# Performance work log

Measured on AMD Instinct MI355X. Metric: run time of the kernel, lower is better.

The kernel has to match this reference:

```python
import jax, jax.numpy as jnp
import numpy as np

TOP_K = 2


def setup_inputs() -> dict:
    key = jax.random.key(0)
    k1, k2, k3, k4, k5 = jax.random.split(key, 5)
    B, S, D, F, E = 2, 2048, 1024, 4096, 8
    hidden_states = jax.random.normal(k1, (B, S, D), dtype=jnp.float32)
    gate_w = jax.random.normal(k2, (E, D), dtype=jnp.float32) / np.sqrt(D)
    w1 = jax.random.normal(k3, (E, F, D), dtype=jnp.float32) / np.sqrt(D)
    w3 = jax.random.normal(k4, (E, F, D), dtype=jnp.float32) / np.sqrt(D)
    w2 = jax.random.normal(k5, (E, D, F), dtype=jnp.float32) / np.sqrt(F)
    return {"hidden_states": hidden_states, "gate_w": gate_w, "w1": w1, "w3": w3, "w2": w2}


def reference(hidden_states, gate_w, w1, w3, w2):
    B, S, D = hidden_states.shape
    E = gate_w.shape[0]
    x = hidden_states.reshape(-1, D)  # [T, D]
    # Router: softmax in float32, top-k, renormalize (Mixtral gating)
    router_logits = x @ gate_w.T  # [T, E]
    probs = jax.nn.softmax(router_logits.astype(jnp.float32), axis=-1)
    routing_weights, selected_experts = jax.lax.top_k(probs, TOP_K)  # [T, K]
    routing_weights = routing_weights / routing_weights.sum(axis=-1, keepdims=True)
    routing_weights = routing_weights.astype(x.dtype)
    out = jnp.zeros_like(x)
    for e in range(E):
        # combined routing weight of expert e for each token (0 if not routed)
        w = (routing_weights * (selected_experts == e)).sum(axis=-1)  # [T]
        h = jax.nn.silu(x @ w1[e].T) * (x @ w3[e].T)  # [T, F]
        out = out + (h @ w2[e].T) * w[:, None]
    return out.reshape(B, S, D)
```

## Files before the change

### kernel.cpp

```cpp
#include <hip/hip_runtime.h>
#include <hip/hip_bf16.h>
#include <stdint.h>

#define T_TOK 4096
#define D_DIM 1024
#define F_DIM 4096
#define E_NUM 8
#define MAXTOK 4096
#define TOTROW 8192

typedef __attribute__((ext_vector_type(8))) short short8;
typedef __attribute__((ext_vector_type(4))) float floatx4;

__device__ __forceinline__ unsigned short f2bf(float f) {
    union { float f; unsigned u; } v; v.f = f;
    unsigned u = v.u;
    u += 0x7fff + ((u >> 16) & 1);
    return (unsigned short)(u >> 16);
}

__device__ __forceinline__ void async_copy16(const unsigned short* g, unsigned short* l) {
    __builtin_amdgcn_global_load_lds(
        (__attribute__((address_space(1))) void*)(g),
        (__attribute__((address_space(3))) void*)(l), 16, 0, 0);
}

__global__ __launch_bounds__(256) void cvt_kernel(
    const float* __restrict__ src, unsigned short* __restrict__ dst, int n8)
{
    int i = blockIdx.x * blockDim.x + threadIdx.x;
    int stride = gridDim.x * blockDim.x;
    for (; i < n8; i += stride) {
        const float4* s = (const float4*)src + 2 * (size_t)i;
        float4 a = s[0], b = s[1];
        short8 o;
        o[0] = (short)f2bf(a.x); o[1] = (short)f2bf(a.y);
        o[2] = (short)f2bf(a.z); o[3] = (short)f2bf(a.w);
        o[4] = (short)f2bf(b.x); o[5] = (short)f2bf(b.y);
        o[6] = (short)f2bf(b.z); o[7] = (short)f2bf(b.w);
        *((short8*)dst + (size_t)i) = o;
    }
}

__global__ __launch_bounds__(64) void router_kernel(
    const float* __restrict__ x, const float* __restrict__ gw,
    int* __restrict__ counts, int* __restrict__ tok, float* __restrict__ rw,
    int* __restrict__ se, int* __restrict__ sp, float* __restrict__ sw)
{
    const int t = blockIdx.x;
    const int l = threadIdx.x;
    const float4* xr = (const float4*)(x + (size_t)t * D_DIM);
    float acc[E_NUM];
#pragma unroll
    for (int e = 0; e < E_NUM; e++) acc[e] = 0.f;
#pragma unroll
    for (int i = 0; i < D_DIM / 4 / 64; i++) {
        float4 xv = xr[l + i * 64];
#pragma unroll
        for (int e = 0; e < E_NUM; e++) {
            float4 gv = ((const float4*)(gw + e * D_DIM))[l + i * 64];
            acc[e] += xv.x * gv.x + xv.y * gv.y + xv.z * gv.z + xv.w * gv.w;
        }
    }
#pragma unroll
    for (int e = 0; e < E_NUM; e++) {
        float a = acc[e];
        for (int off = 32; off > 0; off >>= 1) a += __shfl_xor(a, off, 64);
        acc[e] = a;
    }
    if (l == 0) {
        int e0 = 0;
#pragma unroll
        for (int e = 1; e < E_NUM; e++) if (acc[e] > acc[e0]) e0 = e;
        int e1 = (e0 == 0) ? 1 : 0;
#pragma unroll
        for (int e = 0; e < E_NUM; e++) if (e != e0 && acc[e] > acc[e1]) e1 = e;
        float w0 = 1.f / (1.f + expf(acc[e1] - acc[e0]));
        float w1 = 1.f - w0;
        int p0 = atomicAdd(&counts[e0], 1);
        tok[e0 * MAXTOK + p0] = t; rw[e0 * MAXTOK + p0] = w0;
        int p1 = atomicAdd(&counts[e1], 1);
        tok[e1 * MAXTOK + p1] = t; rw[e1 * MAXTOK + p1] = w1;
        se[2 * t] = e0; sp[2 * t] = p0; sw[2 * t] = w0;
        se[2 * t + 1] = e1; sp[2 * t + 1] = p1; sw[2 * t + 1] = w1;
    }
}

__global__ void prefix_kernel(const int* __restrict__ counts, int* __restrict__ offsets)
{
    if (threadIdx.x == 0 && blockIdx.x == 0) {
        int run = 0;
        for (int e = 0; e < E_NUM; e++) { offsets[e] = run; run += counts[e]; }
    }
}


__global__ __launch_bounds__(256, 4) void gemm1f_kernel(
    const unsigned short* __restrict__ xb,
    const unsigned short* __restrict__ w1b, const unsigned short* __restrict__ w3b,
    const int* __restrict__ counts, const int* __restrict__ offsets,
    const int* __restrict__ tok, unsigned short* __restrict__ h)
{
    const int lin = blockIdx.x + 32 * (blockIdx.y + 64 * blockIdx.z);
    const int w = (lin & 7) * 2048 + (lin >> 3);
    const int tm = w & 31;
    const int tn = (w >> 5) & 63;
    const int e  = w >> 11;

    const int cnt = counts[e];
    if (tm * 128 >= cnt) return;
    const int tid = threadIdx.x;

    __shared__ unsigned short sA[2][128 * 32];
    __shared__ unsigned short sB1[2][64 * 32];
    __shared__ unsigned short sB3[2][64 * 32];
    __shared__ int tokS[128];

    if (tid < 128) {
        int r = tm * 128 + tid;
        tokS[tid] = tok[e * MAXTOK + (r < cnt ? r : cnt - 1)];
    }
    __syncthreads();

    const int wave = tid >> 6, lane = tid & 63;
    const int wx = wave & 1, wy = wave >> 1;
    const int quad = lane >> 4, tl = lane & 15;

    const int sr = tid >> 2;
    const int scw = ((tid & 3) ^ ((sr >> 1) & 3)) * 8;
    const unsigned offA0 = (unsigned)tokS[sr] * D_DIM + scw;
    const unsigned offA1 = (unsigned)tokS[sr + 64] * D_DIM + scw;
    const unsigned offB  = ((unsigned)e * F_DIM + (unsigned)tn * 64 + sr) * D_DIM + scw;

    const int l0 = wave * 512;
    const int l1 = 2048 + wave * 512;

    floatx4 acc1[4][2], acc3[4][2];
#pragma unroll
    for (int a = 0; a < 4; a++)
#pragma unroll
        for (int b = 0; b < 2; b++) {
            acc1[a][b] = (floatx4){0.f, 0.f, 0.f, 0.f};
            acc3[a][b] = (floatx4){0.f, 0.f, 0.f, 0.f};
        }

    async_copy16(xb + offA0, sA[0] + l0);
    async_copy16(xb + offA1, sA[0] + l1);
    async_copy16(w1b + offB, sB1[0] + l0);
    async_copy16(w3b + offB, sB3[0] + l0);
    __syncthreads();

    int cur = 0;
    for (int kk = 0; kk < D_DIM; kk += 32) {
        const int nk = kk + 32;
        if (nk < D_DIM) {
            async_copy16(xb + offA0 + nk, sA[cur ^ 1] + l0);
            async_copy16(xb + offA1 + nk, sA[cur ^ 1] + l1);
            async_copy16(w1b + offB + nk, sB1[cur ^ 1] + l0);
            async_copy16(w3b + offB + nk, sB3[cur ^ 1] + l0);
        }

        short8 af[4];
#pragma unroll
        for (int mt = 0; mt < 4; mt++) {
            const int ra = wy * 64 + mt * 16 + tl;
            af[mt] = *(const short8*)(sA[cur] + ra * 32 + (quad ^ ((ra >> 1) & 3)) * 8);
        }
#pragma unroll
        for (int nt = 0; nt < 2; nt++) {
            const int rb = wx * 32 + nt * 16 + tl;
            const int cb = (quad ^ ((rb >> 1) & 3)) * 8;
            short8 b1 = *(const short8*)(sB1[cur] + rb * 32 + cb);
            short8 b3 = *(const short8*)(sB3[cur] + rb * 32 + cb);
#pragma unroll
            for (int mt = 0; mt < 4; mt++) {
                acc1[mt][nt] = __builtin_amdgcn_mfma_f32_16x16x32_bf16(af[mt], b1, acc1[mt][nt], 0, 0, 0);
                acc3[mt][nt] = __builtin_amdgcn_mfma_f32_16x16x32_bf16(af[mt], b3, acc3[mt][nt], 0, 0, 0);
            }
        }
        __syncthreads();
        cur ^= 1;
    }

    const int hbase = offsets[e];
#pragma unroll
    for (int mt = 0; mt < 4; mt++)
#pragma unroll
        for (int nt = 0; nt < 2; nt++)
#pragma unroll
            for (int i = 0; i < 4; i++) {
                int r = tm * 128 + wy * 64 + mt * 16 + quad * 4 + i;
                if (r < cnt) {
                    int c = tn * 64 + wx * 32 + nt * 16 + tl;
                    float z1 = acc1[mt][nt][i];
                    float z3 = acc3[mt][nt][i];
                    float hv = (z1 / (1.f + expf(-z1))) * z3;
                    h[(size_t)(hbase + r) * F_DIM + c] = f2bf(hv);
                }
            }
}

__global__ __launch_bounds__(256, 4) void gemm2f_kernel(
    const unsigned short* __restrict__ h, const unsigned short* __restrict__ w2b,
    const int* __restrict__ counts, const int* __restrict__ offsets,
    float* __restrict__ hout)
{
    const int lin = blockIdx.x + 32 * (blockIdx.y + 8 * blockIdx.z);
    const int w = (lin & 7) * 256 + (lin >> 3);
    const int tm = w & 31;
    const int tn = (w >> 5) & 7;
    const int e  = w >> 8;

    const int cnt = counts[e];
    if (tm * 128 >= cnt) return;
    const int tid = threadIdx.x;

    __shared__ unsigned short sA[2][128 * 32];
    __shared__ unsigned short sB[2][128 * 32];

    const int hbase = offsets[e];
    const int wave = tid >> 6, lane = tid & 63;
    const int wx = wave & 1, wy = wave >> 1;
    const int quad = lane >> 4, tl = lane & 15;

    const int sr = tid >> 2;
    const int scw = ((tid & 3) ^ ((sr >> 1) & 3)) * 8;
    int ra0 = hbase + tm * 128 + sr;      if (ra0 > TOTROW - 1) ra0 = TOTROW - 1;
    int ra1 = ra0 + 64;                   if (ra1 > TOTROW - 1) ra1 = TOTROW - 1;
    const unsigned offA0 = (unsigned)ra0 * F_DIM + scw;
    const unsigned offA1 = (unsigned)ra1 * F_DIM + scw;
    const unsigned offB  = ((unsigned)e * D_DIM + (unsigned)tn * 128 + sr) * F_DIM + scw;
    const unsigned offB1 = offB + 64u * F_DIM;

    const int l0 = wave * 512;
    const int l1 = 2048 + wave * 512;

    floatx4 acc[4][4];
#pragma unroll
    for (int a = 0; a < 4; a++)
#pragma unroll
        for (int b = 0; b < 4; b++) acc[a][b] = (floatx4){0.f, 0.f, 0.f, 0.f};

    async_copy16(h + offA0, sA[0] + l0);
    async_copy16(h + offA1, sA[0] + l1);
    async_copy16(w2b + offB, sB[0] + l0);
    async_copy16(w2b + offB1, sB[0] + l1);
    __syncthreads();

    int cur = 0;
    for (int kk = 0; kk < F_DIM; kk += 32) {
        const int nk = kk + 32;
        if (nk < F_DIM) {
            async_copy16(h + offA0 + nk, sA[cur ^ 1] + l0);
            async_copy16(h + offA1 + nk, sA[cur ^ 1] + l1);
            async_copy16(w2b + offB + nk, sB[cur ^ 1] + l0);
            async_copy16(w2b + offB1 + nk, sB[cur ^ 1] + l1);
        }

        short8 af[4];
#pragma unroll
        for (int mt = 0; mt < 4; mt++) {
            const int ra = wy * 64 + mt * 16 + tl;
            af[mt] = *(const short8*)(sA[cur] + ra * 32 + (quad ^ ((ra >> 1) & 3)) * 8);
        }
#pragma unroll
        for (int nt = 0; nt < 4; nt++) {
            const int rb = wx * 64 + nt * 16 + tl;
            short8 bf = *(const short8*)(sB[cur] + rb * 32 + (quad ^ ((rb >> 1) & 3)) * 8);
#pragma unroll
            for (int mt = 0; mt < 4; mt++)
                acc[mt][nt] = __builtin_amdgcn_mfma_f32_16x16x32_bf16(af[mt], bf, acc[mt][nt], 0, 0, 0);
        }
        __syncthreads();
        cur ^= 1;
    }

#pragma unroll
    for (int mt = 0; mt < 4; mt++)
#pragma unroll
        for (int nt = 0; nt < 4; nt++)
#pragma unroll
            for (int i = 0; i < 4; i++) {
                int r = tm * 128 + wy * 64 + mt * 16 + quad * 4 + i;
                if (r < cnt) {
                    int c = tn * 128 + wx * 64 + nt * 16 + tl;
                    hout[(size_t)(hbase + r) * D_DIM + c] = acc[mt][nt][i];
                }
            }
}

__global__ __launch_bounds__(256) void combine_kernel(
    const float* __restrict__ hout, const int* __restrict__ offsets,
    const int* __restrict__ se, const int* __restrict__ sp, const float* __restrict__ sw,
    float* __restrict__ out)
{
    const int t = blockIdx.x;
    const int tid = threadIdx.x;
    int s0 = offsets[se[2 * t]] + sp[2 * t];
    int s1 = offsets[se[2 * t + 1]] + sp[2 * t + 1];
    float w0 = sw[2 * t], w1 = sw[2 * t + 1];
    float4 a = ((const float4*)(hout + (size_t)s0 * D_DIM))[tid];
    float4 b = ((const float4*)(hout + (size_t)s1 * D_DIM))[tid];
    float4 o;
    o.x = w0 * a.x + w1 * b.x; o.y = w0 * a.y + w1 * b.y;
    o.z = w0 * a.z + w1 * b.z; o.w = w0 * a.w + w1 * b.w;
    ((float4*)(out + (size_t)t * D_DIM))[tid] = o;
}

#define BM 64
#define BN 64
#define LDSP 40

__global__ __launch_bounds__(256) void gemm1s_kernel(
    const float* __restrict__ x, const float* __restrict__ w1,
    const float* __restrict__ w3,
    const int* __restrict__ counts, const int* __restrict__ offsets,
    const int* __restrict__ tok, unsigned short* __restrict__ h)
{
    const int e = blockIdx.z;
    const int cnt = counts[e];
    const int tm = blockIdx.x;
    if (tm * BM >= cnt) return;
    const int tn = blockIdx.y;
    const int tid = threadIdx.x;

    __shared__ unsigned short As[BM][LDSP];
    __shared__ unsigned short B1s[BN][LDSP];
    __shared__ unsigned short B3s[BN][LDSP];
    __shared__ int tokS[BM];

    if (tid < BM) {
        int r = tm * BM + tid;
        tokS[tid] = (r < cnt) ? tok[e * MAXTOK + r] : -1;
    }
    __syncthreads();

    const int wave = tid >> 6;
    const int lane = tid & 63;
    const int wx = wave & 1, wy = wave >> 1;
    const int quad = lane >> 4, tl = lane & 15;

    floatx4 acc1[2][2], acc3[2][2];
#pragma unroll
    for (int a = 0; a < 2; a++)
#pragma unroll
        for (int b = 0; b < 2; b++) {
            acc1[a][b] = (floatx4){0.f, 0.f, 0.f, 0.f};
            acc3[a][b] = (floatx4){0.f, 0.f, 0.f, 0.f};
        }

    const float* w1e = w1 + (size_t)e * F_DIM * D_DIM + (size_t)(tn * BN) * D_DIM;
    const float* w3e = w3 + (size_t)e * F_DIM * D_DIM + (size_t)(tn * BN) * D_DIM;

    for (int kk = 0; kk < D_DIM; kk += 32) {
#pragma unroll
        for (int i = 0; i < 2; i++) {
            int j = tid + i * 256;
            int r = j >> 3, c4 = j & 7;
            float4 v = make_float4(0.f, 0.f, 0.f, 0.f);
            int tkn = tokS[r];
            if (tkn >= 0) v = *(const float4*)(x + (size_t)tkn * D_DIM + kk + c4 * 4);
            unsigned short* dst = &As[r][c4 * 4];
            dst[0] = f2bf(v.x); dst[1] = f2bf(v.y); dst[2] = f2bf(v.z); dst[3] = f2bf(v.w);
        }
#pragma unroll
        for (int i = 0; i < 2; i++) {
            int j = tid + i * 256;
            int r = j >> 3, c4 = j & 7;
            const float4 v1 = *(const float4*)(w1e + (size_t)r * D_DIM + kk + c4 * 4);
            const float4 v3 = *(const float4*)(w3e + (size_t)r * D_DIM + kk + c4 * 4);
            unsigned short* d1 = &B1s[r][c4 * 4];
            d1[0] = f2bf(v1.x); d1[1] = f2bf(v1.y); d1[2] = f2bf(v1.z); d1[3] = f2bf(v1.w);
            unsigned short* d3 = &B3s[r][c4 * 4];
            d3[0] = f2bf(v3.x); d3[1] = f2bf(v3.y); d3[2] = f2bf(v3.z); d3[3] = f2bf(v3.w);
        }
        __syncthreads();

        short8 a0 = *(const short8*)&As[wy * 32 + tl][quad * 8];
        short8 a1 = *(const short8*)&As[wy * 32 + 16 + tl][quad * 8];
        short8 b1a = *(const short8*)&B1s[wx * 32 + tl][quad * 8];
        short8 b1b = *(const short8*)&B1s[wx * 32 + 16 + tl][quad * 8];
        short8 b3a = *(const short8*)&B3s[wx * 32 + tl][quad * 8];
        short8 b3b = *(const short8*)&B3s[wx * 32 + 16 + tl][quad * 8];

        acc1[0][0] = __builtin_amdgcn_mfma_f32_16x16x32_bf16(a0, b1a, acc1[0][0], 0, 0, 0);
        acc1[0][1] = __builtin_amdgcn_mfma_f32_16x16x32_bf16(a0, b1b, acc1[0][1], 0, 0, 0);
        acc1[1][0] = __builtin_amdgcn_mfma_f32_16x16x32_bf16(a1, b1a, acc1[1][0], 0, 0, 0);
        acc1[1][1] = __builtin_amdgcn_mfma_f32_16x16x32_bf16(a1, b1b, acc1[1][1], 0, 0, 0);
        acc3[0][0] = __builtin_amdgcn_mfma_f32_16x16x32_bf16(a0, b3a, acc3[0][0], 0, 0, 0);
        acc3[0][1] = __builtin_amdgcn_mfma_f32_16x16x32_bf16(a0, b3b, acc3[0][1], 0, 0, 0);
        acc3[1][0] = __builtin_amdgcn_mfma_f32_16x16x32_bf16(a1, b3a, acc3[1][0], 0, 0, 0);
        acc3[1][1] = __builtin_amdgcn_mfma_f32_16x16x32_bf16(a1, b3b, acc3[1][1], 0, 0, 0);
        __syncthreads();
    }

    const int hbase = offsets[e];
#pragma unroll
    for (int mt = 0; mt < 2; mt++)
#pragma unroll
        for (int nt = 0; nt < 2; nt++)
#pragma unroll
            for (int i = 0; i < 4; i++) {
                int rl = wy * 32 + mt * 16 + quad * 4 + i;
                int r = tm * BM + rl;
                if (r < cnt) {
                    int c = tn * BN + wx * 32 + nt * 16 + tl;
                    float z1 = acc1[mt][nt][i];
                    float z3 = acc3[mt][nt][i];
                    float hv = (z1 / (1.f + expf(-z1))) * z3;
                    h[(size_t)(hbase + r) * F_DIM + c] = f2bf(hv);
                }
            }
}

__global__ __launch_bounds__(256) void gemm2s_kernel(
    const unsigned short* __restrict__ h, const float* __restrict__ w2,
    const int* __restrict__ counts, const int* __restrict__ offsets,
    const int* __restrict__ tok, const float* __restrict__ rw,
    float* __restrict__ out)
{
    const int e = blockIdx.z;
    const int cnt = counts[e];
    const int tm = blockIdx.x;
    if (tm * BM >= cnt) return;
    const int tn = blockIdx.y;
    const int tid = threadIdx.x;

    __shared__ unsigned short As[BM][LDSP];
    __shared__ unsigned short Bs[BN][LDSP];
    __shared__ int tokS[BM];
    __shared__ float rwS[BM];

    const int hbase = offsets[e];
    if (tid < BM) {
        int r = tm * BM + tid;
        tokS[tid] = (r < cnt) ? tok[e * MAXTOK + r] : -1;
        rwS[tid] = (r < cnt) ? rw[e * MAXTOK + r] : 0.f;
    }
    __syncthreads();

    const int wave = tid >> 6, lane = tid & 63;
    const int wx = wave & 1, wy = wave >> 1;
    const int quad = lane >> 4, tl = lane & 15;

    floatx4 acc[2][2];
#pragma unroll
    for (int a = 0; a < 2; a++)
#pragma unroll
        for (int b = 0; b < 2; b++) acc[a][b] = (floatx4){0.f, 0.f, 0.f, 0.f};

    const float* w2e = w2 + (size_t)e * D_DIM * F_DIM + (size_t)(tn * BN) * F_DIM;
    const unsigned short* hA = h + (size_t)(hbase + tm * BM) * F_DIM;

    for (int kk = 0; kk < F_DIM; kk += 32) {
        {
            int r = tid >> 2, c8 = tid & 3;
            short8 v = {0, 0, 0, 0, 0, 0, 0, 0};
            if (tm * BM + r < cnt) v = *(const short8*)(hA + (size_t)r * F_DIM + kk + c8 * 8);
            *(short8*)&As[r][c8 * 8] = v;
        }
#pragma unroll
        for (int i = 0; i < 2; i++) {
            int j = tid + i * 256;
            int r = j >> 3, c4 = j & 7;
            const float4 v = *(const float4*)(w2e + (size_t)r * F_DIM + kk + c4 * 4);
            unsigned short* dst = &Bs[r][c4 * 4];
            dst[0] = f2bf(v.x); dst[1] = f2bf(v.y); dst[2] = f2bf(v.z); dst[3] = f2bf(v.w);
        }
        __syncthreads();

        short8 a0 = *(const short8*)&As[wy * 32 + tl][quad * 8];
        short8 a1 = *(const short8*)&As[wy * 32 + 16 + tl][quad * 8];
        short8 b0 = *(const short8*)&Bs[wx * 32 + tl][quad * 8];
        short8 b1 = *(const short8*)&Bs[wx * 32 + 16 + tl][quad * 8];

        acc[0][0] = __builtin_amdgcn_mfma_f32_16x16x32_bf16(a0, b0, acc[0][0], 0, 0, 0);
        acc[0][1] = __builtin_amdgcn_mfma_f32_16x16x32_bf16(a0, b1, acc[0][1], 0, 0, 0);
        acc[1][0] = __builtin_amdgcn_mfma_f32_16x16x32_bf16(a1, b0, acc[1][0], 0, 0, 0);
        acc[1][1] = __builtin_amdgcn_mfma_f32_16x16x32_bf16(a1, b1, acc[1][1], 0, 0, 0);
        __syncthreads();
    }

#pragma unroll
    for (int mt = 0; mt < 2; mt++)
#pragma unroll
        for (int nt = 0; nt < 2; nt++)
#pragma unroll
            for (int i = 0; i < 4; i++) {
                int rl = wy * 32 + mt * 16 + quad * 4 + i;
                int r = tm * BM + rl;
                if (r < cnt) {
                    int t = tokS[rl];
                    float w = rwS[rl];
                    int c = tn * BN + wx * 32 + nt * 16 + tl;
                    atomicAdd(&out[(size_t)t * D_DIM + c], acc[mt][nt][i] * w);
                }
            }
}

extern "C" void kernel_launch(void* const* d_in, const int* in_sizes, int n_in,
                              void* d_out, int out_size, void* d_ws, size_t ws_size,
                              hipStream_t stream)
{
    const float* x  = (const float*)d_in[0];
    const float* gw = (const float*)d_in[1];
    const float* w1 = (const float*)d_in[2];
    const float* w3 = (const float*)d_in[3];
    const float* w2 = (const float*)d_in[4];
    float* out = (float*)d_out;

    char* p = (char*)d_ws;
    int* counts  = (int*)p;            p += 64;
    int* offsets = (int*)p;            p += 64;
    int* tok     = (int*)p;            p += (size_t)E_NUM * MAXTOK * 4;
    float* rw    = (float*)p;          p += (size_t)E_NUM * MAXTOK * 4;

    const size_t SEL = (size_t)2 * T_TOK * 4;
    const size_t XB  = (size_t)T_TOK * D_DIM * 2;
    const size_t WB  = (size_t)E_NUM * F_DIM * D_DIM * 2;
    const size_t HB  = (size_t)TOTROW * F_DIM * 2;
    const size_t HO  = (size_t)TOTROW * D_DIM * 4;
    const size_t small = (size_t)(p - (char*)d_ws);
    const size_t need_fast = small + 3 * SEL + XB + 3 * WB + HB + HO;

    if (ws_size >= need_fast) {
        int* se = (int*)p;               p += SEL;
        int* sp = (int*)p;               p += SEL;
        float* sw = (float*)p;           p += SEL;
        unsigned short* xb  = (unsigned short*)p;  p += XB;
        unsigned short* w1b = (unsigned short*)p;  p += WB;
        unsigned short* w3b = (unsigned short*)p;  p += WB;
        unsigned short* w2b = (unsigned short*)p;  p += WB;
        unsigned short* h   = (unsigned short*)p;  p += HB;
        float* hout = (float*)p;

        hipMemsetAsync(counts, 0, 64, stream);
        cvt_kernel<<<2048, 256, 0, stream>>>(x,  xb,  T_TOK * D_DIM / 8);
        cvt_kernel<<<8192, 256, 0, stream>>>(w1, w1b, E_NUM * F_DIM * D_DIM / 8);
        cvt_kernel<<<8192, 256, 0, stream>>>(w3, w3b, E_NUM * F_DIM * D_DIM / 8);
        cvt_kernel<<<8192, 256, 0, stream>>>(w2, w2b, E_NUM * F_DIM * D_DIM / 8);
        router_kernel<<<T_TOK, 64, 0, stream>>>(x, gw, counts, tok, rw, se, sp, sw);
        prefix_kernel<<<1, 64, 0, stream>>>(counts, offsets);
        dim3 g1(T_TOK / 128, F_DIM / 64, E_NUM);
        gemm1f_kernel<<<g1, 256, 0, stream>>>(xb, w1b, w3b, counts, offsets, tok, h);
        dim3 g2(T_TOK / 128, D_DIM / 128, E_NUM);
        gemm2f_kernel<<<g2, 256, 0, stream>>>(h, w2b, counts, offsets, hout);
        combine_kernel<<<T_TOK, 256, 0, stream>>>(hout, offsets, se, sp, sw, out);
    } else {
        unsigned short* h = (unsigned short*)p;
        int* se = (int*)h;
        int* sp = se + 2 * T_TOK;
        float* sw = (float*)(sp + 2 * T_TOK);

        hipMemsetAsync(counts, 0, 64, stream);
        hipMemsetAsync(d_out, 0, (size_t)out_size * sizeof(float), stream);
        router_kernel<<<T_TOK, 64, 0, stream>>>(x, gw, counts, tok, rw, se, sp, sw);
        prefix_kernel<<<1, 64, 0, stream>>>(counts, offsets);
        dim3 g1(T_TOK / BM, F_DIM / BN, E_NUM);
        gemm1s_kernel<<<g1, 256, 0, stream>>>(x, w1, w3, counts, offsets, tok, h);
        dim3 g2(T_TOK / BM, D_DIM / BN, E_NUM);
        gemm2s_kernel<<<g2, 256, 0, stream>>>(h, w2, counts, offsets, tok, rw, out);
    }
}
```

Baseline: 866.4 us.

## Fuse fp32-to-bf16 weight conversion into expert GEMM tile loads

Removes the three standalone conversion kernels that turned w1, w3 and w2 into bf16 copies in workspace. The GEMM kernels now read fp32 weight tiles into registers, convert them with packed bf16 conversions, and write them to LDS after the MFMA work of the current step, which keeps the double-buffer prefetch. This avoids a full extra read and write pass over all expert weights. In exchange, each weight tile is fetched as fp32 by every token tile of the expert, so global traffic per GEMM grows and depends on cache reuse. gemm2 also moves to 64-wide N tiles, and gemm1 lowers its occupancy hint.

```diff
diff --git a/kernel.cpp b/kernel.cpp
--- a/kernel.cpp
+++ b/kernel.cpp
@@ -17,6 +17,17 @@
     unsigned u = v.u;
     u += 0x7fff + ((u >> 16) & 1);
     return (unsigned short)(u >> 16);
+}
+
+__device__ __forceinline__ unsigned pk2(float lo, float hi) {
+    __hip_bfloat162 r = __float22bfloat162_rn(make_float2(lo, hi));
+    return *reinterpret_cast<unsigned*>(&r);
+}
+__device__ __forceinline__ short8 cvt8(float4 a, float4 b) {
+    union { unsigned u[4]; short8 s; } o;
+    o.u[0] = pk2(a.x, a.y); o.u[1] = pk2(a.z, a.w);
+    o.u[2] = pk2(b.x, b.y); o.u[3] = pk2(b.z, b.w);
+    return o.s;
 }
 
 __device__ __forceinline__ void async_copy16(const unsigned short* g, unsigned short* l) {
@@ -95,9 +106,9 @@
 }
 
 
-__global__ __launch_bounds__(256, 4) void gemm1f_kernel(
+__global__ __launch_bounds__(256, 3) void gemm1f_kernel(
     const unsigned short* __restrict__ xb,
-    const unsigned short* __restrict__ w1b, const unsigned short* __restrict__ w3b,
+    const float* __restrict__ w1, const float* __restrict__ w3,
     const int* __restrict__ counts, const int* __restrict__ offsets,
     const int* __restrict__ tok, unsigned short* __restrict__ h)
 {
@@ -127,10 +138,13 @@
     const int quad = lane >> 4, tl = lane & 15;
 
     const int sr = tid >> 2;
-    const int scw = ((tid & 3) ^ ((sr >> 1) & 3)) * 8;
-    const unsigned offA0 = (unsigned)tokS[sr] * D_DIM + scw;
-    const unsigned offA1 = (unsigned)tokS[sr + 64] * D_DIM + scw;
-    const unsigned offB  = ((unsigned)e * F_DIM + (unsigned)tn * 64 + sr) * D_DIM + scw;
+    const int swz = ((tid & 3) ^ ((sr >> 1) & 3)) * 8;
+    const unsigned offA0 = (unsigned)tokS[sr] * D_DIM + swz;
+    const unsigned offA1 = (unsigned)tokS[sr + 64] * D_DIM + swz;
+    const unsigned browB = ((unsigned)e * F_DIM + (unsigned)tn * 64 + sr) * D_DIM + swz;
+    const float4* gB1 = (const float4*)(w1 + browB);
+    const float4* gB3 = (const float4*)(w3 + browB);
+    const int dstB = tid * 8;
 
     const int l0 = wave * 512;
     const int l1 = 2048 + wave * 512;
@@ -144,20 +158,26 @@
             acc3[a][b] = (floatx4){0.f, 0.f, 0.f, 0.f};
         }
 
-    async_copy16(xb + offA0, sA[0] + l0);
-    async_copy16(xb + offA1, sA[0] + l1);
-    async_copy16(w1b + offB, sB1[0] + l0);
-    async_copy16(w3b + offB, sB3[0] + l0);
+    {
+        float4 p1a = gB1[0], p1b = gB1[1];
+        float4 p3a = gB3[0], p3b = gB3[1];
+        async_copy16(xb + offA0, sA[0] + l0);
+        async_copy16(xb + offA1, sA[0] + l1);
+        *(short8*)(sB1[0] + dstB) = cvt8(p1a, p1b);
+        *(short8*)(sB3[0] + dstB) = cvt8(p3a, p3b);
+    }
     __syncthreads();
 
     int cur = 0;
     for (int kk = 0; kk < D_DIM; kk += 32) {
         const int nk = kk + 32;
-        if (nk < D_DIM) {
+        const bool pf = nk < D_DIM;
+        float4 p1a, p1b, p3a, p3b;
+        if (pf) {
+            p1a = gB1[nk / 4]; p1b = gB1[nk / 4 + 1];
+            p3a = gB3[nk / 4]; p3b = gB3[nk / 4 + 1];
             async_copy16(xb + offA0 + nk, sA[cur ^ 1] + l0);
             async_copy16(xb + offA1 + nk, sA[cur ^ 1] + l1);
-            async_copy16(w1b + offB + nk, sB1[cur ^ 1] + l0);
-            async_copy16(w3b + offB + nk, sB3[cur ^ 1] + l0);
         }
 
         short8 af[4];
@@ -177,6 +197,10 @@
                 acc1[mt][nt] = __builtin_amdgcn_mfma_f32_16x16x32_bf16(af[mt], b1, acc1[mt][nt], 0, 0, 0);
                 acc3[mt][nt] = __builtin_amdgcn_mfma_f32_16x16x32_bf16(af[mt], b3, acc3[mt][nt], 0, 0, 0);
             }
+        }
+        if (pf) {
+            *(short8*)(sB1[cur ^ 1] + dstB) = cvt8(p1a, p1b);
+            *(short8*)(sB3[cur ^ 1] + dstB) = cvt8(p3a, p3b);
         }
         __syncthreads();
         cur ^= 1;
@@ -201,22 +225,22 @@
 }
 
 __global__ __launch_bounds__(256, 4) void gemm2f_kernel(
-    const unsigned short* __restrict__ h, const unsigned short* __restrict__ w2b,
+    const unsigned short* __restrict__ h, const float* __restrict__ w2,
     const int* __restrict__ counts, const int* __restrict__ offsets,
     float* __restrict__ hout)
 {
-    const int lin = blockIdx.x + 32 * (blockIdx.y + 8 * blockIdx.z);
-    const int w = (lin & 7) * 256 + (lin >> 3);
+    const int lin = blockIdx.x + 32 * (blockIdx.y + 16 * blockIdx.z);
+    const int w = (lin & 7) * 512 + (lin >> 3);
     const int tm = w & 31;
-    const int tn = (w >> 5) & 7;
-    const int e  = w >> 8;
+    const int tn = (w >> 5) & 15;
+    const int e  = w >> 9;
 
     const int cnt = counts[e];
     if (tm * 128 >= cnt) return;
     const int tid = threadIdx.x;
 
     __shared__ unsigned short sA[2][128 * 32];
-    __shared__ unsigned short sB[2][128 * 32];
+    __shared__ unsigned short sB[2][64 * 32];
 
     const int hbase = offsets[e];
     const int wave = tid >> 6, lane = tid & 63;
@@ -224,37 +248,41 @@
     const int quad = lane >> 4, tl = lane & 15;
 
     const int sr = tid >> 2;
-    const int scw = ((tid & 3) ^ ((sr >> 1) & 3)) * 8;
+    const int swz = ((tid & 3) ^ ((sr >> 1) & 3)) * 8;
     int ra0 = hbase + tm * 128 + sr;      if (ra0 > TOTROW - 1) ra0 = TOTROW - 1;
     int ra1 = ra0 + 64;                   if (ra1 > TOTROW - 1) ra1 = TOTROW - 1;
-    const unsigned offA0 = (unsigned)ra0 * F_DIM + scw;
-    const unsigned offA1 = (unsigned)ra1 * F_DIM + scw;
-    const unsigned offB  = ((unsigned)e * D_DIM + (unsigned)tn * 128 + sr) * F_DIM + scw;
-    const unsigned offB1 = offB + 64u * F_DIM;
+    const unsigned offA0 = (unsigned)ra0 * F_DIM + swz;
+    const unsigned offA1 = (unsigned)ra1 * F_DIM + swz;
+    const unsigned browB = ((unsigned)e * D_DIM + (unsigned)tn * 64 + sr) * F_DIM + swz;
+    const float4* gB = (const float4*)(w2 + browB);
+    const int dstB = tid * 8;
 
     const int l0 = wave * 512;
     const int l1 = 2048 + wave * 512;
 
-    floatx4 acc[4][4];
+    floatx4 acc[4][2];
 #pragma unroll
     for (int a = 0; a < 4; a++)
 #pragma unroll
-        for (int b = 0; b < 4; b++) acc[a][b] = (floatx4){0.f, 0.f, 0.f, 0.f};
-
-    async_copy16(h + offA0, sA[0] + l0);
-    async_copy16(h + offA1, sA[0] + l1);
-    async_copy16(w2b + offB, sB[0] + l0);
-    async_copy16(w2b + offB1, sB[0] + l1);
+        for (int b = 0; b < 2; b++) acc[a][b] = (floatx4){0.f, 0.f, 0.f, 0.f};
+
+    {
+        float4 pa = gB[0], pb = gB[1];
+        async_copy16(h + offA0, sA[0] + l0);
+        async_copy16(h + offA1, sA[0] + l1);
+        *(short8*)(sB[0] + dstB) = cvt8(pa, pb);
+    }
     __syncthreads();
 
     int cur = 0;
     for (int kk = 0; kk < F_DIM; kk += 32) {
         const int nk = kk + 32;
-        if (nk < F_DIM) {
+        const bool pf = nk < F_DIM;
+        float4 pa, pb;
+        if (pf) {
+            pa = gB[nk / 4]; pb = gB[nk / 4 + 1];
             async_copy16(h + offA0 + nk, sA[cur ^ 1] + l0);
             async_copy16(h + offA1 + nk, sA[cur ^ 1] + l1);
-            async_copy16(w2b + offB + nk, sB[cur ^ 1] + l0);
-            async_copy16(w2b + offB1 + nk, sB[cur ^ 1] + l1);
         }
 
         short8 af[4];
@@ -264,13 +292,16 @@
             af[mt] = *(const short8*)(sA[cur] + ra * 32 + (quad ^ ((ra >> 1) & 3)) * 8);
         }
 #pragma unroll
-        for (int nt = 0; nt < 4; nt++) {
-            const int rb = wx * 64 + nt * 16 + tl;
+        for (int nt = 0; nt < 2; nt++) {
+            const int rb = wx * 32 + nt * 16 + tl;
             short8 bf = *(const short8*)(sB[cur] + rb * 32 + (quad ^ ((rb >> 1) & 3)) * 8);
 #pragma unroll
             for (int mt = 0; mt < 4; mt++)
                 acc[mt][nt] = __builtin_amdgcn_mfma_f32_16x16x32_bf16(af[mt], bf, acc[mt][nt], 0, 0, 0);
         }
+        if (pf) {
+            *(short8*)(sB[cur ^ 1] + dstB) = cvt8(pa, pb);
+        }
         __syncthreads();
         cur ^= 1;
     }
@@ -278,12 +309,12 @@
 #pragma unroll
     for (int mt = 0; mt < 4; mt++)
 #pragma unroll
-        for (int nt = 0; nt < 4; nt++)
+        for (int nt = 0; nt < 2; nt++)
 #pragma unroll
             for (int i = 0; i < 4; i++) {
                 int r = tm * 128 + wy * 64 + mt * 16 + quad * 4 + i;
                 if (r < cnt) {
-                    int c = tn * 128 + wx * 64 + nt * 16 + tl;
+                    int c = tn * 64 + wx * 32 + nt * 16 + tl;
                     hout[(size_t)(hbase + r) * D_DIM + c] = acc[mt][nt][i];
                 }
             }
@@ -517,34 +548,27 @@
 
     const size_t SEL = (size_t)2 * T_TOK * 4;
     const size_t XB  = (size_t)T_TOK * D_DIM * 2;
-    const size_t WB  = (size_t)E_NUM * F_DIM * D_DIM * 2;
     const size_t HB  = (size_t)TOTROW * F_DIM * 2;
     const size_t HO  = (size_t)TOTROW * D_DIM * 4;
     const size_t small = (size_t)(p - (char*)d_ws);
-    const size_t need_fast = small + 3 * SEL + XB + 3 * WB + HB + HO;
+    const size_t need_fast = small + 3 * SEL + XB + HB + HO;
 
     if (ws_size >= need_fast) {
         int* se = (int*)p;               p += SEL;
         int* sp = (int*)p;               p += SEL;
         float* sw = (float*)p;           p += SEL;
         unsigned short* xb  = (unsigned short*)p;  p += XB;
-        unsigned short* w1b = (unsigned short*)p;  p += WB;
-        unsigned short* w3b = (unsigned short*)p;  p += WB;
-        unsigned short* w2b = (unsigned short*)p;  p += WB;
         unsigned short* h   = (unsigned short*)p;  p += HB;
         float* hout = (float*)p;
 
         hipMemsetAsync(counts, 0, 64, stream);
-        cvt_kernel<<<2048, 256, 0, stream>>>(x,  xb,  T_TOK * D_DIM / 8);
-        cvt_kernel<<<8192, 256, 0, stream>>>(w1, w1b, E_NUM * F_DIM * D_DIM / 8);
-        cvt_kernel<<<8192, 256, 0, stream>>>(w3, w3b, E_NUM * F_DIM * D_DIM / 8);
-        cvt_kernel<<<8192, 256, 0, stream>>>(w2, w2b, E_NUM * F_DIM * D_DIM / 8);
+        cvt_kernel<<<2048, 256, 0, stream>>>(x, xb, T_TOK * D_DIM / 8);
         router_kernel<<<T_TOK, 64, 0, stream>>>(x, gw, counts, tok, rw, se, sp, sw);
         prefix_kernel<<<1, 64, 0, stream>>>(counts, offsets);
         dim3 g1(T_TOK / 128, F_DIM / 64, E_NUM);
-        gemm1f_kernel<<<g1, 256, 0, stream>>>(xb, w1b, w3b, counts, offsets, tok, h);
-        dim3 g2(T_TOK / 128, D_DIM / 128, E_NUM);
-        gemm2f_kernel<<<g2, 256, 0, stream>>>(h, w2b, counts, offsets, hout);
+        gemm1f_kernel<<<g1, 256, 0, stream>>>(xb, w1, w3, counts, offsets, tok, h);
+        dim3 g2(T_TOK / 128, D_DIM / 64, E_NUM);
+        gemm2f_kernel<<<g2, 256, 0, stream>>>(h, w2, counts, offsets, hout);
         combine_kernel<<<T_TOK, 256, 0, stream>>>(hout, offsets, se, sp, sw, out);
     } else {
         unsigned short* h = (unsigned short*)p;
```

New measurement: 1.029 ms. 18.8% more time.

## Fuse combine into expert down-proj via atomic scatter, merge conversion kernels

Applied to the files above, without the earlier changes.

The down-projection kernel now scales each row by its routing weight and atomically adds it into the output token row, removing the intermediate per-slot output buffer and the separate combine kernel. The x bf16 conversion moves into the router kernel, and the three weight conversions merge into one launch. This cuts launches and intermediate memory traffic, at the cost of fp32 atomics, non-deterministic summation order, and a memset of the output.

```diff
diff --git a/kernel.cpp b/kernel.cpp
--- a/kernel.cpp
+++ b/kernel.cpp
@@ -25,27 +25,34 @@
         (__attribute__((address_space(3))) void*)(l), 16, 0, 0);
 }
 
-__global__ __launch_bounds__(256) void cvt_kernel(
-    const float* __restrict__ src, unsigned short* __restrict__ dst, int n8)
-{
-    int i = blockIdx.x * blockDim.x + threadIdx.x;
-    int stride = gridDim.x * blockDim.x;
-    for (; i < n8; i += stride) {
-        const float4* s = (const float4*)src + 2 * (size_t)i;
-        float4 a = s[0], b = s[1];
-        short8 o;
-        o[0] = (short)f2bf(a.x); o[1] = (short)f2bf(a.y);
-        o[2] = (short)f2bf(a.z); o[3] = (short)f2bf(a.w);
-        o[4] = (short)f2bf(b.x); o[5] = (short)f2bf(b.y);
-        o[6] = (short)f2bf(b.z); o[7] = (short)f2bf(b.w);
-        *((short8*)dst + (size_t)i) = o;
+__global__ __launch_bounds__(256) void cvtw_kernel(
+    const float* __restrict__ s1, unsigned short* __restrict__ d1,
+    const float* __restrict__ s3, unsigned short* __restrict__ d3,
+    const float* __restrict__ s2, unsigned short* __restrict__ d2, int n8)
+{
+    const int stride = gridDim.x * blockDim.x;
+    const int base = blockIdx.x * blockDim.x + threadIdx.x;
+#pragma unroll
+    for (int t = 0; t < 3; t++) {
+        const float* src = (t == 0) ? s1 : (t == 1) ? s3 : s2;
+        unsigned short* dst = (t == 0) ? d1 : (t == 1) ? d3 : d2;
+        for (int i = base; i < n8; i += stride) {
+            const float4* s = (const float4*)src + 2 * (size_t)i;
+            float4 a = s[0], b = s[1];
+            short8 o;
+            o[0] = (short)f2bf(a.x); o[1] = (short)f2bf(a.y);
+            o[2] = (short)f2bf(a.z); o[3] = (short)f2bf(a.w);
+            o[4] = (short)f2bf(b.x); o[5] = (short)f2bf(b.y);
+            o[6] = (short)f2bf(b.z); o[7] = (short)f2bf(b.w);
+            *((short8*)dst + (size_t)i) = o;
+        }
     }
 }
 
 __global__ __launch_bounds__(64) void router_kernel(
     const float* __restrict__ x, const float* __restrict__ gw,
     int* __restrict__ counts, int* __restrict__ tok, float* __restrict__ rw,
-    int* __restrict__ se, int* __restrict__ sp, float* __restrict__ sw)
+    unsigned short* __restrict__ xb)
 {
     const int t = blockIdx.x;
     const int l = threadIdx.x;
@@ -56,6 +63,10 @@
 #pragma unroll
     for (int i = 0; i < D_DIM / 4 / 64; i++) {
         float4 xv = xr[l + i * 64];
+        union { unsigned short q[4]; uint2 u; } pk;
+        pk.q[0] = f2bf(xv.x); pk.q[1] = f2bf(xv.y);
+        pk.q[2] = f2bf(xv.z); pk.q[3] = f2bf(xv.w);
+        ((uint2*)(xb + (size_t)t * D_DIM))[l + i * 64] = pk.u;
 #pragma unroll
         for (int e = 0; e < E_NUM; e++) {
             float4 gv = ((const float4*)(gw + e * D_DIM))[l + i * 64];
@@ -81,8 +92,6 @@
         tok[e0 * MAXTOK + p0] = t; rw[e0 * MAXTOK + p0] = w0;
         int p1 = atomicAdd(&counts[e1], 1);
         tok[e1 * MAXTOK + p1] = t; rw[e1 * MAXTOK + p1] = w1;
-        se[2 * t] = e0; sp[2 * t] = p0; sw[2 * t] = w0;
-        se[2 * t + 1] = e1; sp[2 * t + 1] = p1; sw[2 * t + 1] = w1;
     }
 }
 
@@ -203,7 +212,8 @@
 __global__ __launch_bounds__(256, 4) void gemm2f_kernel(
     const unsigned short* __restrict__ h, const unsigned short* __restrict__ w2b,
     const int* __restrict__ counts, const int* __restrict__ offsets,
-    float* __restrict__ hout)
+    const int* __restrict__ tok, const float* __restrict__ rw,
+    float* __restrict__ out)
 {
     const int lin = blockIdx.x + 32 * (blockIdx.y + 8 * blockIdx.z);
     const int w = (lin & 7) * 256 + (lin >> 3);
@@ -217,8 +227,18 @@
 
     __shared__ unsigned short sA[2][128 * 32];
     __shared__ unsigned short sB[2][128 * 32];
+    __shared__ int tokS[128];
+    __shared__ float rwS[128];
 
     const int hbase = offsets[e];
+    if (tid < 128) {
+        int r = tm * 128 + tid;
+        bool v = r < cnt;
+        tokS[tid] = tok[e * MAXTOK + (v ? r : cnt - 1)];
+        rwS[tid] = v ? rw[e * MAXTOK + r] : 0.f;
+    }
+    __syncthreads();
+
     const int wave = tid >> 6, lane = tid & 63;
     const int wx = wave & 1, wy = wave >> 1;
     const int quad = lane >> 4, tl = lane & 15;
@@ -281,30 +301,13 @@
         for (int nt = 0; nt < 4; nt++)
 #pragma unroll
             for (int i = 0; i < 4; i++) {
-                int r = tm * 128 + wy * 64 + mt * 16 + quad * 4 + i;
+                int rl = wy * 64 + mt * 16 + quad * 4 + i;
+                int r = tm * 128 + rl;
                 if (r < cnt) {
                     int c = tn * 128 + wx * 64 + nt * 16 + tl;
-                    hout[(size_t)(hbase + r) * D_DIM + c] = acc[mt][nt][i];
+                    atomicAdd(&out[(size_t)tokS[rl] * D_DIM + c], acc[mt][nt][i] * rwS[rl]);
                 }
             }
-}
-
-__global__ __launch_bounds__(256) void combine_kernel(
-    const float* __restrict__ hout, const int* __restrict__ offsets,
-    const int* __restrict__ se, const int* __restrict__ sp, const float* __restrict__ sw,
-    float* __restrict__ out)
-{
-    const int t = blockIdx.x;
-    const int tid = threadIdx.x;
-    int s0 = offsets[se[2 * t]] + sp[2 * t];
-    int s1 = offsets[se[2 * t + 1]] + sp[2 * t + 1];
-    float w0 = sw[2 * t], w1 = sw[2 * t + 1];
-    float4 a = ((const float4*)(hout + (size_t)s0 * D_DIM))[tid];
-    float4 b = ((const float4*)(hout + (size_t)s1 * D_DIM))[tid];
-    float4 o;
-    o.x = w0 * a.x + w1 * b.x; o.y = w0 * a.y + w1 * b.y;
-    o.z = w0 * a.z + w1 * b.z; o.w = w0 * a.w + w1 * b.w;
-    ((float4*)(out + (size_t)t * D_DIM))[tid] = o;
 }
 
 #define BM 64
@@ -515,46 +518,35 @@
     int* tok     = (int*)p;            p += (size_t)E_NUM * MAXTOK * 4;
     float* rw    = (float*)p;          p += (size_t)E_NUM * MAXTOK * 4;
 
-    const size_t SEL = (size_t)2 * T_TOK * 4;
     const size_t XB  = (size_t)T_TOK * D_DIM * 2;
     const size_t WB  = (size_t)E_NUM * F_DIM * D_DIM * 2;
     const size_t HB  = (size_t)TOTROW * F_DIM * 2;
-    const size_t HO  = (size_t)TOTROW * D_DIM * 4;
     const size_t small = (size_t)(p - (char*)d_ws);
-    const size_t need_fast = small + 3 * SEL + XB + 3 * WB + HB + HO;
+    const size_t need_fast = small + XB + 3 * WB + HB;
 
     if (ws_size >= need_fast) {
-        int* se = (int*)p;               p += SEL;
-        int* sp = (int*)p;               p += SEL;
-        float* sw = (float*)p;           p += SEL;
         unsigned short* xb  = (unsigned short*)p;  p += XB;
         unsigned short* w1b = (unsigned short*)p;  p += WB;
         unsigned short* w3b = (unsigned short*)p;  p += WB;
         unsigned short* w2b = (unsigned short*)p;  p += WB;
         unsigned short* h   = (unsigned short*)p;  p += HB;
-        float* hout = (float*)p;
 
         hipMemsetAsync(counts, 0, 64, stream);
-        cvt_kernel<<<2048, 256, 0, stream>>>(x,  xb,  T_TOK * D_DIM / 8);
-        cvt_kernel<<<8192, 256, 0, stream>>>(w1, w1b, E_NUM * F_DIM * D_DIM / 8);
-        cvt_kernel<<<8192, 256, 0, stream>>>(w3, w3b, E_NUM * F_DIM * D_DIM / 8);
-        cvt_kernel<<<8192, 256, 0, stream>>>(w2, w2b, E_NUM * F_DIM * D_DIM / 8);
-        router_kernel<<<T_TOK, 64, 0, stream>>>(x, gw, counts, tok, rw, se, sp, sw);
+        hipMemsetAsync(d_out, 0, (size_t)out_size * sizeof(float), stream);
+        cvtw_kernel<<<8192, 256, 0, stream>>>(w1, w1b, w3, w3b, w2, w2b,
+                                              E_NUM * F_DIM * D_DIM / 8);
+        router_kernel<<<T_TOK, 64, 0, stream>>>(x, gw, counts, tok, rw, xb);
         prefix_kernel<<<1, 64, 0, stream>>>(counts, offsets);
         dim3 g1(T_TOK / 128, F_DIM / 64, E_NUM);
         gemm1f_kernel<<<g1, 256, 0, stream>>>(xb, w1b, w3b, counts, offsets, tok, h);
         dim3 g2(T_TOK / 128, D_DIM / 128, E_NUM);
-        gemm2f_kernel<<<g2, 256, 0, stream>>>(h, w2b, counts, offsets, hout);
-        combine_kernel<<<T_TOK, 256, 0, stream>>>(hout, offsets, se, sp, sw, out);
+        gemm2f_kernel<<<g2, 256, 0, stream>>>(h, w2b, counts, offsets, tok, rw, out);
     } else {
         unsigned short* h = (unsigned short*)p;
-        int* se = (int*)h;
-        int* sp = se + 2 * T_TOK;
-        float* sw = (float*)(sp + 2 * T_TOK);
 
         hipMemsetAsync(counts, 0, 64, stream);
         hipMemsetAsync(d_out, 0, (size_t)out_size * sizeof(float), stream);
-        router_kernel<<<T_TOK, 64, 0, stream>>>(x, gw, counts, tok, rw, se, sp, sw);
+        router_kernel<<<T_TOK, 64, 0, stream>>>(x, gw, counts, tok, rw, h);
         prefix_kernel<<<1, 64, 0, stream>>>(counts, offsets);
         dim3 g1(T_TOK / BM, F_DIM / BN, E_NUM);
         gemm1s_kernel<<<g1, 256, 0, stream>>>(x, w1, w3, counts, offsets, tok, h);
```

After: 877.6 us. About the same (+1.3%).
